# Performance work log

Hardware: AMD Instinct MI355X
Metric: run time of the kernel (lower is better)

## Reference

```python
import jax, jax.numpy as jnp
import numpy as np

B, N, E, D = 8, 4096, 65536, 256


def setup_inputs() -> dict:
    key = jax.random.key(0)
    ks = jax.random.split(key, 4)
    return {
        "node_features": jax.random.normal(ks[0], (B, N, D), dtype=jnp.float32),
        "W": jax.random.normal(ks[1], (D, D), dtype=jnp.float32) * (1.0 / np.sqrt(D)),
        "b": jnp.zeros((D,), dtype=jnp.float32),
        "gamma": jnp.ones((D,), dtype=jnp.float32),
        "beta": jnp.zeros((D,), dtype=jnp.float32),
        "edge_index": jax.random.randint(ks[2], (B, 2, E), 0, N, dtype=jnp.int64),
        "node_mask": jax.random.randint(ks[3], (B, N), 0, 2, dtype=jnp.int32),
    }


def reference(node_features, W, b, gamma, beta, edge_index, node_mask):
    # Linear projection: h = x @ W^T + b   (nn.Linear convention, W: [out, in])
    h = jnp.einsum("bni,oi->bno", node_features, W) + b  # [B, N, D]
    batch, n_nodes, d = h.shape
    n_edges = edge_index.shape[2]

    src = edge_index[:, 0, :]  # [B, E]
    tgt = edge_index[:, 1, :]  # [B, E]

    nm = node_mask.astype(h.dtype)  # [B, N]
    # edge valid iff both endpoints are valid nodes
    emask = jnp.take_along_axis(nm, src, axis=1) * jnp.take_along_axis(nm, tgt, axis=1)  # [B, E]

    # gather source features, mask invalid edges
    msg = jnp.take_along_axis(h, src[..., None], axis=1) * emask[..., None]  # [B, E, D]

    # batched scatter-add via flat segment_sum with per-batch offsets
    seg_ids = (tgt + jnp.arange(batch, dtype=tgt.dtype)[:, None] * n_nodes).reshape(-1)
    agg = jax.ops.segment_sum(msg.reshape(batch * n_edges, d), seg_ids,
                              num_segments=batch * n_nodes).reshape(batch, n_nodes, d)

    h = h + agg / jnp.sqrt(jnp.asarray(n_nodes, h.dtype))

    # dropout is identity in eval mode
    # LayerNorm over last dim (eps = 1e-5, torch default)
    mu = jnp.mean(h, axis=-1, keepdims=True)
    var = jnp.mean((h - mu) ** 2, axis=-1, keepdims=True)
    h = (h - mu) * jax.lax.rsqrt(var + 1e-5) * gamma + beta

    h = jax.nn.relu(h)
    return h * nm[..., None]
```

## Files before the change

### kernel.cpp

```cpp
#include <hip/hip_runtime.h>
#include <hip/hip_bf16.h>

#define NN 4096
#define DIM 256
#define NE 65536
#define TOT_NODES 32768
#define TOT_EDGES 524288

__device__ __forceinline__ float ldf(const void* p, int isbf, size_t i) {
    return isbf ? __bfloat162float(((const __hip_bfloat16*)p)[i]) : ((const float*)p)[i];
}
__device__ __forceinline__ int ldi(const void* p, int is64, size_t i) {
    return is64 ? (int)((const long long*)p)[i] : ((const int*)p)[i];
}

__global__ __launch_bounds__(256)
void init_detect_kernel(const void* ei, const void* nm, const void* x,
                        int* __restrict__ flags, int* __restrict__ counts)
{
    const int t = threadIdx.x;
    counts[blockIdx.x * 256 + t] = 0;
    if (blockIdx.x == 0 && t < 64) {
        const long long ev = ((const long long*)ei)[t];
        const unsigned long long okE = __ballot(ev >= 0 && ev < NN);
        const long long mv = ((const long long*)nm)[t];
        const unsigned long long okM = __ballot(mv == 0 || mv == 1);
        const unsigned int w = ((const unsigned int*)x)[t];
        const int e = (w >> 7) & 0xFF;
        const unsigned long long okF = __ballot(e >= 100 && e <= 140);
        if (t == 0) {
            flags[0] = (okE == ~0ULL) ? 1 : 0;
            flags[1] = (okM == ~0ULL) ? 1 : 0;
            flags[2] = (__popcll(okF) >= 40) ? 1 : 0;
        }
    }
}


typedef __attribute__((ext_vector_type(8))) __bf16 bf16x8;
typedef __attribute__((ext_vector_type(4))) float  f32x4;

__device__ __forceinline__ unsigned short f2bf(float f) {
    unsigned u = __float_as_uint(f);
    u = (u + 0x7fffu + ((u >> 16) & 1u)) >> 16;
    return (unsigned short)u;
}
__device__ __forceinline__ float bf2f(unsigned short h) {
    return __uint_as_float(((unsigned)h) << 16);
}
__device__ __forceinline__ void cvt_hilo(float4 f, ushort4* hi, ushort4* lo) {
    const unsigned short h0 = f2bf(f.x), h1 = f2bf(f.y), h2 = f2bf(f.z), h3 = f2bf(f.w);
    *hi = make_ushort4(h0, h1, h2, h3);
    *lo = make_ushort4(f2bf(f.x - bf2f(h0)), f2bf(f.y - bf2f(h1)),
                       f2bf(f.z - bf2f(h2)), f2bf(f.w - bf2f(h3)));
}
__device__ __forceinline__ bf16x8 frag_ld(const unsigned short* base, int row, int col) {
    const int byte = ((row * 64 + col) * 2) ^ ((row & 7) << 4);
    return *(const bf16x8*)((const char*)base + byte);
}
__device__ __forceinline__ void gload16(const void* g, void* l) {
    __builtin_amdgcn_global_load_lds(
        (const __attribute__((address_space(1))) unsigned int*)g,
        (__attribute__((address_space(3))) unsigned int*)l, 16, 0, 0);
}

__global__ __launch_bounds__(512)
void gemm_kernel(const void* __restrict__ x, const void* __restrict__ w,
                 const void* __restrict__ bias, const int* __restrict__ flags,
                 float* __restrict__ h)
{
    __shared__ unsigned short As[2][128 * 64];
    __shared__ unsigned short Bs[2][256 * 64];

    const int fbf = flags[2];
    const int t = threadIdx.x;
    const int lane = t & 63;
    const int wid = t >> 6;
    const int wr = wid >> 2;
    const int wc = wid & 3;
    const int m0 = (int)blockIdx.x * 128;

    f32x4 acc[4][4];
#pragma unroll
    for (int mi = 0; mi < 4; ++mi)
#pragma unroll
        for (int nj = 0; nj < 4; ++nj)
            acc[mi][nj] = (f32x4){0.f, 0.f, 0.f, 0.f};

    const int lr = lane & 15;
    const int lk8 = (lane >> 4) << 3;

    auto compute_hh = [&](const unsigned short* Ab, const unsigned short* Bb) {
#pragma unroll
        for (int kk = 0; kk < 64; kk += 32) {
            const int lk = kk + lk8;
            bf16x8 aH[4], bH[4];
#pragma unroll
            for (int mi = 0; mi < 4; ++mi)
                aH[mi] = frag_ld(Ab, wr * 64 + mi * 16 + lr, lk);
#pragma unroll
            for (int nj = 0; nj < 4; ++nj)
                bH[nj] = frag_ld(Bb, wc * 64 + nj * 16 + lr, lk);
#pragma unroll
            for (int mi = 0; mi < 4; ++mi)
#pragma unroll
                for (int nj = 0; nj < 4; ++nj)
                    acc[mi][nj] = __builtin_amdgcn_mfma_f32_16x16x32_bf16(
                        aH[mi], bH[nj], acc[mi][nj], 0, 0, 0);
        }
    };

    if (fbf) {
        const unsigned short* xp = (const unsigned short*)x;
        const unsigned short* wp = (const unsigned short*)w;
        auto stage = [&](int kt, int buf) {
            const int k0 = kt * 64;
#pragma unroll
            for (int i = 0; i < 2; ++i) {
                const int s = i * 512 + t;
                const int row = s >> 3, cg = (s & 7) ^ (row & 7);
                gload16(xp + (size_t)(m0 + row) * 256 + k0 + cg * 8, &As[buf][s * 8]);
            }
#pragma unroll
            for (int i = 0; i < 4; ++i) {
                const int s = i * 512 + t;
                const int row = s >> 3, cg = (s & 7) ^ (row & 7);
                gload16(wp + (size_t)row * 256 + k0 + cg * 8, &Bs[buf][s * 8]);
            }
        };
        stage(0, 0);
        for (int kt = 0; kt < 4; ++kt) {
            __syncthreads();
            if (kt < 3) stage(kt + 1, (kt + 1) & 1);
            compute_hh(As[kt & 1], Bs[kt & 1]);
        }
    } else {
        const float* xp = (const float*)x;
        const float* wp = (const float*)w;
        for (int kt = 0; kt < 4; ++kt) {
            const int k0 = kt * 64;
#pragma unroll
            for (int i = 0; i < 2; ++i) {
                const int s = i * 512 + t;
                const int row = s >> 3, cg = (s & 7) ^ (row & 7);
                const float* src = xp + (size_t)(m0 + row) * 256 + k0 + cg * 8;
                const float4 f0 = *(const float4*)src, f1 = *(const float4*)(src + 4);
                ushort4 h0, l0, h1, l1;
                cvt_hilo(f0, &h0, &l0); cvt_hilo(f1, &h1, &l1);
                *(ushort4*)&As[0][s * 8]     = h0; *(ushort4*)&As[0][s * 8 + 4] = h1;
                *(ushort4*)&As[1][s * 8]     = l0; *(ushort4*)&As[1][s * 8 + 4] = l1;
            }
#pragma unroll
            for (int i = 0; i < 4; ++i) {
                const int s = i * 512 + t;
                const int row = s >> 3, cg = (s & 7) ^ (row & 7);
                const float* src = wp + (size_t)row * 256 + k0 + cg * 8;
                const float4 f0 = *(const float4*)src, f1 = *(const float4*)(src + 4);
                ushort4 h0, l0, h1, l1;
                cvt_hilo(f0, &h0, &l0); cvt_hilo(f1, &h1, &l1);
                *(ushort4*)&Bs[0][s * 8]     = h0; *(ushort4*)&Bs[0][s * 8 + 4] = h1;
                *(ushort4*)&Bs[1][s * 8]     = l0; *(ushort4*)&Bs[1][s * 8 + 4] = l1;
            }
            __syncthreads();
            compute_hh(As[0], Bs[0]);
#pragma unroll
            for (int kk = 0; kk < 64; kk += 32) {
                const int lk = kk + lk8;
                bf16x8 aH[4], bH[4], aL[4], bL[4];
#pragma unroll
                for (int mi = 0; mi < 4; ++mi) {
                    aH[mi] = frag_ld(As[0], wr * 64 + mi * 16 + lr, lk);
                    aL[mi] = frag_ld(As[1], wr * 64 + mi * 16 + lr, lk);
                }
#pragma unroll
                for (int nj = 0; nj < 4; ++nj) {
                    bH[nj] = frag_ld(Bs[0], wc * 64 + nj * 16 + lr, lk);
                    bL[nj] = frag_ld(Bs[1], wc * 64 + nj * 16 + lr, lk);
                }
#pragma unroll
                for (int mi = 0; mi < 4; ++mi)
#pragma unroll
                    for (int nj = 0; nj < 4; ++nj) {
                        acc[mi][nj] = __builtin_amdgcn_mfma_f32_16x16x32_bf16(
                            aH[mi], bL[nj], acc[mi][nj], 0, 0, 0);
                        acc[mi][nj] = __builtin_amdgcn_mfma_f32_16x16x32_bf16(
                            aL[mi], bH[nj], acc[mi][nj], 0, 0, 0);
                    }
            }
            __syncthreads();
        }
    }

    const int r4 = (lane >> 4) << 2;
#pragma unroll
    for (int nj = 0; nj < 4; ++nj) {
        const int n = wc * 64 + nj * 16 + lr;
        const float bv = ldf(bias, fbf, n);
#pragma unroll
        for (int mi = 0; mi < 4; ++mi) {
            const int rb = m0 + wr * 64 + mi * 16 + r4;
#pragma unroll
            for (int r = 0; r < 4; ++r)
                h[(size_t)(rb + r) * 256 + n] = acc[mi][nj][r] + bv;
        }
    }
}

__global__ __launch_bounds__(256)
void count_kernel(const void* __restrict__ ei, const void* __restrict__ nm,
                  const int* __restrict__ flags, int* __restrict__ counts)
{
    const int e64 = flags[0], m64 = flags[1];
    const int tid = blockIdx.x * 256 + threadIdx.x;
    const int b = tid >> 15;
    const int k = (tid & 32767) << 1;
    const size_t eb = (size_t)b * 2 * NE;
    int s0, s1, t0, t1;
    if (e64) {
        const longlong2 sv = *(const longlong2*)((const long long*)ei + eb + k);
        const longlong2 tv = *(const longlong2*)((const long long*)ei + eb + NE + k);
        s0 = (int)sv.x; s1 = (int)sv.y; t0 = (int)tv.x; t1 = (int)tv.y;
    } else {
        const int2 sv = *(const int2*)((const int*)ei + eb + k);
        const int2 tv = *(const int2*)((const int*)ei + eb + NE + k);
        s0 = sv.x; s1 = sv.y; t0 = tv.x; t1 = tv.y;
    }
    const size_t mb = (size_t)b * NN;
    if (ldi(nm, m64, mb + s0) && ldi(nm, m64, mb + t0))
        atomicAdd(&counts[b * NN + t0], 1);
    if (ldi(nm, m64, mb + s1) && ldi(nm, m64, mb + t1))
        atomicAdd(&counts[b * NN + t1], 1);
}

__global__ __launch_bounds__(256)
void scan_kernel(int* __restrict__ counts, int* __restrict__ offsets)
{
    __shared__ int sums[256];
    const int t = threadIdx.x;
    int s = 0;
    for (int i = 0; i < 128; ++i) s += counts[i * 256 + t];
    sums[t] = s;
    __syncthreads();
    for (int off = 1; off < 256; off <<= 1) {
        int v = (t >= off) ? sums[t - off] : 0;
        __syncthreads();
        sums[t] += v;
        __syncthreads();
    }
    int run = sums[t] - s;
    for (int i = 0; i < 128; ++i) {
        const int idx = i * 256 + t;
        const int c = counts[idx];
        offsets[idx] = run;
        counts[idx] = run;
        run += c;
    }
}

__global__ __launch_bounds__(256)
void fill_kernel(const void* __restrict__ ei, const void* __restrict__ nm,
                 const int* __restrict__ flags,
                 int* __restrict__ cursor, int* __restrict__ bucket)
{
    const int e64 = flags[0], m64 = flags[1];
    const int tid = blockIdx.x * 256 + threadIdx.x;
    const int b = tid >> 15;
    const int k = (tid & 32767) << 1;
    const size_t eb = (size_t)b * 2 * NE;
    int s0, s1, t0, t1;
    if (e64) {
        const longlong2 sv = *(const longlong2*)((const long long*)ei + eb + k);
        const longlong2 tv = *(const longlong2*)((const long long*)ei + eb + NE + k);
        s0 = (int)sv.x; s1 = (int)sv.y; t0 = (int)tv.x; t1 = (int)tv.y;
    } else {
        const int2 sv = *(const int2*)((const int*)ei + eb + k);
        const int2 tv = *(const int2*)((const int*)ei + eb + NE + k);
        s0 = sv.x; s1 = sv.y; t0 = tv.x; t1 = tv.y;
    }
    const size_t mb = (size_t)b * NN;
    if (ldi(nm, m64, mb + s0) && ldi(nm, m64, mb + t0))
        bucket[atomicAdd(&cursor[b * NN + t0], 1)] = s0;
    if (ldi(nm, m64, mb + s1) && ldi(nm, m64, mb + t1))
        bucket[atomicAdd(&cursor[b * NN + t1], 1)] = s1;
}

__global__ __launch_bounds__(256)
void node_kernel(const float* __restrict__ h, const int* __restrict__ offsets,
                 const int* __restrict__ ends, const int* __restrict__ bucket,
                 const void* __restrict__ nm, const int* __restrict__ flags,
                 const void* __restrict__ gamma, const void* __restrict__ beta,
                 void* __restrict__ out)
{
    const int blk = ((blockIdx.x & 7) << 10) | (blockIdx.x >> 3);
    const int bt = blk * 4 + (threadIdx.x >> 6);
    const int lane = threadIdx.x & 63;
    const int m64 = flags[1], fbf = flags[2];
    const size_t o4 = (size_t)bt * 64 + lane;
    if (!ldi(nm, m64, bt)) {
        if (fbf) ((ushort4*)out)[o4] = make_ushort4(0, 0, 0, 0);
        else     ((float4*)out)[o4]  = make_float4(0.f, 0.f, 0.f, 0.f);
        return;
    }
    const int b = bt >> 12;
    const float4* hb = (const float4*)h + ((size_t)b << 12) * 64;
    const float4 self = ((const float4*)h)[o4];
    const int s0 = offsets[bt], s1 = ends[bt];
    float4 a0 = make_float4(0.f, 0.f, 0.f, 0.f), a1 = a0, a2 = a0, a3 = a0;
    int j = s0;
    for (; j + 4 <= s1; j += 4) {
        const float4 v0 = hb[(size_t)bucket[j]     * 64 + lane];
        const float4 v1 = hb[(size_t)bucket[j + 1] * 64 + lane];
        const float4 v2 = hb[(size_t)bucket[j + 2] * 64 + lane];
        const float4 v3 = hb[(size_t)bucket[j + 3] * 64 + lane];
        a0.x += v0.x; a0.y += v0.y; a0.z += v0.z; a0.w += v0.w;
        a1.x += v1.x; a1.y += v1.y; a1.z += v1.z; a1.w += v1.w;
        a2.x += v2.x; a2.y += v2.y; a2.z += v2.z; a2.w += v2.w;
        a3.x += v3.x; a3.y += v3.y; a3.z += v3.z; a3.w += v3.w;
    }
    for (; j < s1; ++j) {
        const float4 v = hb[(size_t)bucket[j] * 64 + lane];
        a0.x += v.x; a0.y += v.y; a0.z += v.z; a0.w += v.w;
    }
    float4 acc;
    acc.x = self.x + ((a0.x + a1.x) + (a2.x + a3.x)) * 0.015625f;
    acc.y = self.y + ((a0.y + a1.y) + (a2.y + a3.y)) * 0.015625f;
    acc.z = self.z + ((a0.z + a1.z) + (a2.z + a3.z)) * 0.015625f;
    acc.w = self.w + ((a0.w + a1.w) + (a2.w + a3.w)) * 0.015625f;

    float v1r = (acc.x + acc.y) + (acc.z + acc.w);
    float v2r = (acc.x * acc.x + acc.y * acc.y) + (acc.z * acc.z + acc.w * acc.w);
#pragma unroll
    for (int off = 32; off > 0; off >>= 1) {
        v1r += __shfl_xor(v1r, off, 64);
        v2r += __shfl_xor(v2r, off, 64);
    }
    const float mu  = v1r * (1.f / 256.f);
    const float var = v2r * (1.f / 256.f) - mu * mu;
    const float inv = rsqrtf(var + 1e-5f);
    const int d0 = lane * 4;
    float y0 = (acc.x - mu) * inv * ldf(gamma, fbf, d0)     + ldf(beta, fbf, d0);
    float y1 = (acc.y - mu) * inv * ldf(gamma, fbf, d0 + 1) + ldf(beta, fbf, d0 + 1);
    float y2 = (acc.z - mu) * inv * ldf(gamma, fbf, d0 + 2) + ldf(beta, fbf, d0 + 2);
    float y3 = (acc.w - mu) * inv * ldf(gamma, fbf, d0 + 3) + ldf(beta, fbf, d0 + 3);
    y0 = fmaxf(y0, 0.f); y1 = fmaxf(y1, 0.f); y2 = fmaxf(y2, 0.f); y3 = fmaxf(y3, 0.f);
    if (fbf) ((ushort4*)out)[o4] = make_ushort4(f2bf(y0), f2bf(y1), f2bf(y2), f2bf(y3));
    else     ((float4*)out)[o4]  = make_float4(y0, y1, y2, y3);
}

static float g_sentinel[256];

extern "C" void kernel_launch(void* const* d_in, const int* in_sizes, int n_in,
                              void* d_out, int out_size, void* d_ws, size_t ws_size,
                              hipStream_t stream)
{
    (void)in_sizes; (void)n_in; (void)out_size;
    const void* x     = d_in[0];
    const void* W     = d_in[1];
    const void* bias  = d_in[2];
    const void* gamma = d_in[3];
    const void* beta  = d_in[4];
    const void* ei    = d_in[5];
    const void* nm    = d_in[6];

    char* ws = (char*)d_ws;
    int* flags   = (int*)ws;
    int* counts  = (int*)(ws + 256);
    int* offsets = (int*)(ws + 131328);
    int* bucket  = (int*)(ws + 262656);
    float* h     = (float*)(ws + 2359808);

    int fail = 0;
    hipGetLastError();
#define CHK(stage) do { if (!fail && hipGetLastError() != hipSuccess) fail = (stage); } while (0)

    init_detect_kernel<<<TOT_NODES / 256, 256, 0, stream>>>(ei, nm, x, flags, counts); CHK(1);
    gemm_kernel<<<TOT_NODES / 128, 512, 0, stream>>>(x, W, bias, flags, h);            CHK(2);
    count_kernel<<<TOT_EDGES / 512, 256, 0, stream>>>(ei, nm, flags, counts);          CHK(3);
    scan_kernel<<<1, 256, 0, stream>>>(counts, offsets);                               CHK(4);
    fill_kernel<<<TOT_EDGES / 512, 256, 0, stream>>>(ei, nm, flags, counts, bucket);   CHK(5);
    node_kernel<<<TOT_NODES / 4, 256, 0, stream>>>(h, offsets, counts, bucket, nm,
                                                   flags, gamma, beta, d_out);         CHK(6);
#undef CHK

    if (fail) {
        for (int i = 0; i < 256; ++i) g_sentinel[i] = 10000.f * (float)fail;
        hipMemcpyAsync(d_out, g_sentinel, sizeof(g_sentinel),
                       hipMemcpyHostToDevice, stream);
    }
}
```

Baseline: 158.0 us.

## Gather neighbor features from bf16 copy and parallelize scan per batch

The GEMM epilogue now writes a second bf16 copy of the projected features. The aggregation kernel gathers neighbor rows from that copy, which halves the bytes of the random gather traffic, while the self term still comes from the fp32 copy. Separately, the prefix scan is split into 8 blocks, one per batch, each offset by b*NE, replacing a single-block serial scan. The cost is extra writes in the GEMM epilogue and a loss of precision in the aggregated messages.

```diff
diff --git a/kernel.cpp b/kernel.cpp
--- a/kernel.cpp
+++ b/kernel.cpp
@@ -67,7 +67,7 @@
 __global__ __launch_bounds__(512)
 void gemm_kernel(const void* __restrict__ x, const void* __restrict__ w,
                  const void* __restrict__ bias, const int* __restrict__ flags,
-                 float* __restrict__ h)
+                 float* __restrict__ h, unsigned short* __restrict__ hb16)
 {
     __shared__ unsigned short As[2][128 * 64];
     __shared__ unsigned short Bs[2][256 * 64];
@@ -200,8 +200,12 @@
         for (int mi = 0; mi < 4; ++mi) {
             const int rb = m0 + wr * 64 + mi * 16 + r4;
 #pragma unroll
-            for (int r = 0; r < 4; ++r)
-                h[(size_t)(rb + r) * 256 + n] = acc[mi][nj][r] + bv;
+            for (int r = 0; r < 4; ++r) {
+                const float v = acc[mi][nj][r] + bv;
+                const size_t idx = (size_t)(rb + r) * 256 + n;
+                h[idx] = v;
+                hb16[idx] = f2bf(v);
+            }
         }
     }
 }
@@ -236,9 +240,12 @@
 void scan_kernel(int* __restrict__ counts, int* __restrict__ offsets)
 {
     __shared__ int sums[256];
+    const int b = blockIdx.x;
     const int t = threadIdx.x;
+    const int base = b * NN;
     int s = 0;
-    for (int i = 0; i < 128; ++i) s += counts[i * 256 + t];
+#pragma unroll
+    for (int i = 0; i < 16; ++i) s += counts[base + i * 256 + t];
     sums[t] = s;
     __syncthreads();
     for (int off = 1; off < 256; off <<= 1) {
@@ -247,9 +254,10 @@
         sums[t] += v;
         __syncthreads();
     }
-    int run = sums[t] - s;
-    for (int i = 0; i < 128; ++i) {
-        const int idx = i * 256 + t;
+    int run = b * NE + sums[t] - s;
+#pragma unroll
+    for (int i = 0; i < 16; ++i) {
+        const int idx = base + i * 256 + t;
         const int c = counts[idx];
         offsets[idx] = run;
         counts[idx] = run;
@@ -285,7 +293,8 @@
 }
 
 __global__ __launch_bounds__(256)
-void node_kernel(const float* __restrict__ h, const int* __restrict__ offsets,
+void node_kernel(const float* __restrict__ h, const unsigned short* __restrict__ hb16,
+                 const int* __restrict__ offsets,
                  const int* __restrict__ ends, const int* __restrict__ bucket,
                  const void* __restrict__ nm, const int* __restrict__ flags,
                  const void* __restrict__ gamma, const void* __restrict__ beta,
@@ -302,24 +311,24 @@
         return;
     }
     const int b = bt >> 12;
-    const float4* hb = (const float4*)h + ((size_t)b << 12) * 64;
+    const ushort4* hg = (const ushort4*)hb16 + ((size_t)b << 12) * 64;
     const float4 self = ((const float4*)h)[o4];
     const int s0 = offsets[bt], s1 = ends[bt];
     float4 a0 = make_float4(0.f, 0.f, 0.f, 0.f), a1 = a0, a2 = a0, a3 = a0;
     int j = s0;
     for (; j + 4 <= s1; j += 4) {
-        const float4 v0 = hb[(size_t)bucket[j]     * 64 + lane];
-        const float4 v1 = hb[(size_t)bucket[j + 1] * 64 + lane];
-        const float4 v2 = hb[(size_t)bucket[j + 2] * 64 + lane];
-        const float4 v3 = hb[(size_t)bucket[j + 3] * 64 + lane];
-        a0.x += v0.x; a0.y += v0.y; a0.z += v0.z; a0.w += v0.w;
-        a1.x += v1.x; a1.y += v1.y; a1.z += v1.z; a1.w += v1.w;
-        a2.x += v2.x; a2.y += v2.y; a2.z += v2.z; a2.w += v2.w;
-        a3.x += v3.x; a3.y += v3.y; a3.z += v3.z; a3.w += v3.w;
+        const ushort4 u0 = hg[(size_t)bucket[j]     * 64 + lane];
+        const ushort4 u1 = hg[(size_t)bucket[j + 1] * 64 + lane];
+        const ushort4 u2 = hg[(size_t)bucket[j + 2] * 64 + lane];
+        const ushort4 u3 = hg[(size_t)bucket[j + 3] * 64 + lane];
+        a0.x += bf2f(u0.x); a0.y += bf2f(u0.y); a0.z += bf2f(u0.z); a0.w += bf2f(u0.w);
+        a1.x += bf2f(u1.x); a1.y += bf2f(u1.y); a1.z += bf2f(u1.z); a1.w += bf2f(u1.w);
+        a2.x += bf2f(u2.x); a2.y += bf2f(u2.y); a2.z += bf2f(u2.z); a2.w += bf2f(u2.w);
+        a3.x += bf2f(u3.x); a3.y += bf2f(u3.y); a3.z += bf2f(u3.z); a3.w += bf2f(u3.w);
     }
     for (; j < s1; ++j) {
-        const float4 v = hb[(size_t)bucket[j] * 64 + lane];
-        a0.x += v.x; a0.y += v.y; a0.z += v.z; a0.w += v.w;
+        const ushort4 u = hg[(size_t)bucket[j] * 64 + lane];
+        a0.x += bf2f(u.x); a0.y += bf2f(u.y); a0.z += bf2f(u.z); a0.w += bf2f(u.w);
     }
     float4 acc;
     acc.x = self.x + ((a0.x + a1.x) + (a2.x + a3.x)) * 0.015625f;
@@ -368,18 +377,19 @@
     int* offsets = (int*)(ws + 131328);
     int* bucket  = (int*)(ws + 262656);
     float* h     = (float*)(ws + 2359808);
+    unsigned short* hb16 = (unsigned short*)(ws + 35914240);
 
     int fail = 0;
     hipGetLastError();
 #define CHK(stage) do { if (!fail && hipGetLastError() != hipSuccess) fail = (stage); } while (0)
 
     init_detect_kernel<<<TOT_NODES / 256, 256, 0, stream>>>(ei, nm, x, flags, counts); CHK(1);
-    gemm_kernel<<<TOT_NODES / 128, 512, 0, stream>>>(x, W, bias, flags, h);            CHK(2);
+    gemm_kernel<<<TOT_NODES / 128, 512, 0, stream>>>(x, W, bias, flags, h, hb16);      CHK(2);
     count_kernel<<<TOT_EDGES / 512, 256, 0, stream>>>(ei, nm, flags, counts);          CHK(3);
-    scan_kernel<<<1, 256, 0, stream>>>(counts, offsets);                               CHK(4);
+    scan_kernel<<<8, 256, 0, stream>>>(counts, offsets);                               CHK(4);
     fill_kernel<<<TOT_EDGES / 512, 256, 0, stream>>>(ei, nm, flags, counts, bucket);   CHK(5);
-    node_kernel<<<TOT_NODES / 4, 256, 0, stream>>>(h, offsets, counts, bucket, nm,
-                                                   flags, gamma, beta, d_out);         CHK(6);
+    node_kernel<<<TOT_NODES / 4, 256, 0, stream>>>(h, hb16, offsets, counts, bucket,
+                                                   nm, flags, gamma, beta, d_out);     CHK(6);
 #undef CHK
 
     if (fail) {
```

Result: no change. 155.9 us (-1.3%).
